# Kernel tuning notes

Hardware: AMD Instinct MI355X
Metric: run time of the kernel (lower is better)

## Reference

```python
import jax, jax.numpy as jnp
import numpy as np

CONF_THRES = 0.5
IOU_THRES = 0.4
MAX_DET = 100
MAX_WH = 1024.0
K_NMS = 4096  # static cap on NMS candidates (>> expected #candidates passing conf_thres)


def setup_inputs() -> dict:
    key = jax.random.key(0)
    k1, k2, k3, k4 = jax.random.split(key, 4)
    bs, gs, nc = 16, 25200, 80  # YOLOv5 @ 640x640: 25200 anchors, 80 classes, ps = 85
    xy = jax.random.uniform(k1, (bs, gs, 2)) * 608.0 + 16.0   # centers in [16, 624)
    wh = jax.random.uniform(k2, (bs, gs, 2)) * 96.0 + 4.0     # sizes in [4, 100)
    obj = jax.random.uniform(k3, (bs, gs, 1))                 # objectness
    cls = jax.random.uniform(k4, (bs, gs, nc)) * 0.505        # class probs; obj*cls > 0.5 is rare (~1-2k hits)
    prediction = jnp.concatenate([xy, wh, obj, cls], axis=-1)  # [bs, gs, 85]
    return {"prediction": prediction}


def _postprocess(prediction):
    bs, gs, ps = prediction.shape
    nc = ps - 5
    p = prediction.reshape(-1, ps)                 # [N, ps], N = bs*gs
    obj = p[:, 4]                                  # objectness
    scores_all = p[:, 5:] * obj[:, None]           # conf = cls * obj, [N, nc]
    # candidate (anchor, class) pairs: obj > conf_thres AND conf > conf_thres (multi_label)
    cand = (obj[:, None] > CONF_THRES) & (scores_all > CONF_THRES)
    flat = jnp.where(cand, scores_all, -1.0).reshape(-1)       # [N*nc]
    top_scores, top_idx = jax.lax.top_k(flat, K_NMS)           # descending score order (= torch nms sort order)
    row = top_idx // nc                                        # anchor index into p
    cls_j = top_idx % nc                                       # class index
    batch = row // gs                                          # image index
    valid = top_scores > CONF_THRES

    # xywh -> xyxy
    xywh = p[row, :4]                                          # [K, 4]
    half = xywh[:, 2:4] * 0.5
    box = jnp.concatenate([xywh[:, 0:2] - half, xywh[:, 0:2] + half], axis=1)
    f32 = box.dtype

    # class-offset + batch-offset trick: c1 = batch*max_cls_idx*max_wh, c2 = class*max_wh
    offset = (batch.astype(f32) * (nc * MAX_WH) + cls_j.astype(f32) * MAX_WH)[:, None]
    nb = box + offset                                          # offset boxes for NMS

    # pairwise IoU [K, K]
    area = (nb[:, 2] - nb[:, 0]) * (nb[:, 3] - nb[:, 1])
    ix = jnp.maximum(jnp.minimum(nb[:, None, 2], nb[None, :, 2]) - jnp.maximum(nb[:, None, 0], nb[None, :, 0]), 0.0)
    iy = jnp.maximum(jnp.minimum(nb[:, None, 3], nb[None, :, 3]) - jnp.maximum(nb[:, None, 1], nb[None, :, 1]), 0.0)
    inter = ix * iy
    iou = inter / (area[:, None] + area[None, :] - inter)

    # greedy NMS over score-sorted candidates (torchvision semantics: suppress if IoU > thres)
    def step(supp, xs):
        iou_i, v_i, i = xs
        keep_i = v_i & jnp.logical_not(supp[i])
        supp = supp | (keep_i & (iou_i > IOU_THRES))
        return supp, keep_i
    _, keep = jax.lax.scan(step, jnp.zeros(K_NMS, bool), (iou, valid, jnp.arange(K_NMS)))

    # output rows: [x1, y1, x2, y2, conf, class, batch]
    rows7 = jnp.concatenate(
        [box, top_scores[:, None], cls_j.astype(f32)[:, None], batch.astype(f32)[:, None]], axis=1)

    # per-image gather of kept rows (score order), truncated to MAX_DET, zero-padded
    def gather_b(b):
        m = keep & (batch == b)
        rank = jnp.cumsum(m.astype(jnp.int32)) - 1
        idx = jnp.where(m & (rank < MAX_DET), rank, MAX_DET)   # overflow/invalid -> dropped slot
        buf = jnp.zeros((MAX_DET + 1, 7), f32).at[idx].set(jnp.where(m[:, None], rows7, 0.0))
        return buf[:MAX_DET]
    return jax.vmap(gather_b)(jnp.arange(bs))                  # [bs, MAX_DET, 7]


def reference(prediction):
    return _postprocess(prediction)
```

## Files before the change

kernel.cpp:

```cpp
#include <hip/hip_runtime.h>
#include <stdint.h>

#define BS 16
#define GS 25200
#define NC 80
#define PS 85
#define NROWS (BS * GS)
#define MAXDET 100
#define CAP 4096
#define NGROUPS (BS * NC)
#define RPB 64
#define SLABF (RPB * PS)
#define PPB (RPB * NC)

struct Ws {
  int      count;
  int      keep[CAP];
  float    sc[CAP];
  int      ti[CAP];
  uint16_t gg[CAP];
  float    x1[CAP];
  float    y1[CAP];
  float    x2[CAP];
  float    y2[CAP];
};

__global__ __launch_bounds__(256) void extract_k(const float* __restrict__ p,
                                                 Ws* __restrict__ w) {
  __shared__ float slab[SLABF];
  int tid = threadIdx.x;
  const float4* __restrict__ src =
      (const float4*)(p + (size_t)blockIdx.x * SLABF);
  float4* dst = (float4*)slab;
#pragma unroll
  for (int i = 0; i < 6; ++i) {
    int idx = tid + i * 256;
    if (idx < SLABF / 4) dst[idx] = src[idx];
  }
  __syncthreads();
  int lane = tid & 63;
  int rowbase = blockIdx.x * RPB;
#pragma unroll 4
  for (int step = 0; step < PPB / 256; ++step) {
    int k = tid + step * 256;
    int row = k / NC;
    int c   = k - row * NC;
    float obj = slab[row * PS + 4];
    bool hit = false;
    float s = 0.0f;
    if (obj > 0.5f) {
      s = slab[row * PS + 5 + c] * obj;
      hit = s > 0.5f;
    }
    uint64_t mm = __ballot(hit);
    if (mm) {
      int leader = __ffsll((unsigned long long)mm) - 1;
      int pos0;
      if (lane == leader) pos0 = atomicAdd(&w->count, __popcll(mm));
      pos0 = __shfl(pos0, leader);
      if (hit) {
        int slot = pos0 + __popcll(mm & ((1ull << lane) - 1ull));
        if (slot < CAP) {
          int grow = rowbase + row;
          int b = grow / GS;
          float x = slab[row * PS + 0], y = slab[row * PS + 1];
          float hw = slab[row * PS + 2] * 0.5f, hh = slab[row * PS + 3] * 0.5f;
          w->sc[slot] = s;
          w->ti[slot] = grow * NC + c;
          w->gg[slot] = (uint16_t)(b * NC + c);
          w->x1[slot] = x - hw;
          w->y1[slot] = y - hh;
          w->x2[slot] = x + hw;
          w->y2[slot] = y + hh;
        }
      }
    }
  }
}

__global__ __launch_bounds__(256) void nms_k(Ws* __restrict__ w) {
  __shared__ uint64_t lkey[4][64];
  __shared__ int      lj[4][64];
  int wslot = threadIdx.x >> 6;
  int wid   = (blockIdx.x * 256 + threadIdx.x) >> 6;
  int lane  = threadIdx.x & 63;
  int b = wid / NC, c = wid - b * NC;
  float offf = (float)b * (NC * 1024.0f) + (float)c * 1024.0f;
  int n = w->count;
  if (n > CAP) n = CAP;
  int nm = 0;
  for (int j0 = 0; j0 < n; j0 += 64) {
    int j = j0 + lane;
    int g = (j < n) ? (int)w->gg[j] : -1;
    bool mem = (g == wid);
    uint64_t mm = __ballot(mem);
    if (!mm) continue;
    if (mem) {
      int pos = nm + __popcll(mm & ((1ull << lane) - 1ull));
      if (pos < 64) {
        uint32_t sb = __float_as_uint(w->sc[j]);
        lkey[wslot][pos] = ((uint64_t)sb << 32) | (uint32_t)(~(uint32_t)w->ti[j]);
        lj[wslot][pos]   = j;
      } else {
        w->keep[j] = 0;
      }
    }
    nm += __popcll(mm);
  }
  __syncthreads();
  if (nm > 64) nm = 64;
  if (nm == 0) return;
  uint64_t key = (lane < nm) ? lkey[wslot][lane] : 0ull;
  int      jv  = (lane < nm) ? lj[wslot][lane] : -1;
  for (int k = 2; k <= 64; k <<= 1) {
    for (int s = k >> 1; s > 0; s >>= 1) {
      uint64_t ok = __shfl_xor(key, s);
      int      oj = __shfl_xor(jv, s);
      bool iLow       = (lane & s) == 0;
      bool descRun    = (lane & k) == 0;
      bool wantLarger = (iLow == descRun);
      bool take = wantLarger ? (ok > key) : (ok < key);
      if (take) { key = ok; jv = oj; }
    }
  }
  float kx1 = 0.f, ky1 = 0.f, kx2 = 0.f, ky2 = 0.f, ka = 0.f;
  int nk = 0;
  for (int i = 0; i < nm; ++i) {
    int jm = __shfl(jv, i);
    float cx1 = w->x1[jm] + offf;
    float cy1 = w->y1[jm] + offf;
    float cx2 = w->x2[jm] + offf;
    float cy2 = w->y2[jm] + offf;
    float car = (cx2 - cx1) * (cy2 - cy1);
    bool over = false;
    if (lane < nk) {
      float ix = fmaxf(fminf(kx2, cx2) - fmaxf(kx1, cx1), 0.0f);
      float iy = fmaxf(fminf(ky2, cy2) - fmaxf(ky1, cy1), 0.0f);
      float inter = ix * iy;
      over = inter / (ka + car - inter) > 0.4f;
    }
    bool kept = !__any(over);
    if (kept) {
      if (lane == nk) { kx1 = cx1; ky1 = cy1; kx2 = cx2; ky2 = cy2; ka = car; }
      ++nk;
    }
    if (lane == 0) w->keep[jm] = kept ? 1 : 0;
  }
}

__global__ __launch_bounds__(1024) void gather_k(const Ws* __restrict__ w,
                                                 float* __restrict__ out) {
  __shared__ uint64_t skey[BS][256];
  __shared__ int      sj[BS][256];
  int wvb  = threadIdx.x >> 6;
  int lane = threadIdx.x & 63;
  int glo = wvb * NC;
  int n = w->count;
  if (n > CAP) n = CAP;
  int nkept = 0;
  for (int j0 = 0; j0 < n; j0 += 64) {
    int j = j0 + lane;
    bool m = false;
    if (j < n) {
      int g = (int)w->gg[j];
      m = ((unsigned)(g - glo) < (unsigned)NC) && (w->keep[j] != 0);
    }
    uint64_t mm = __ballot(m);
    if (m) {
      int pos = nkept + __popcll(mm & ((1ull << lane) - 1ull));
      if (pos < 256) {
        uint32_t sb = __float_as_uint(w->sc[j]);
        skey[wvb][pos] = ((uint64_t)sb << 32) | (uint32_t)(~(uint32_t)w->ti[j]);
        sj[wvb][pos]   = j;
      }
    }
    nkept += __popcll(mm);
  }
  if (nkept > 256) nkept = 256;
  for (int e = lane; e < 256; e += 64)
    if (e >= nkept) { skey[wvb][e] = 0ull; sj[wvb][e] = -1; }
  __syncthreads();
  for (int k = 2; k <= 256; k <<= 1) {
    for (int s = k >> 1; s > 0; s >>= 1) {
      for (int e = lane; e < 256; e += 64) {
        int x = e ^ s;
        if (x > e) {
          uint64_t a = skey[wvb][e], bb = skey[wvb][x];
          bool desc = (e & k) == 0;
          if (desc ? (a < bb) : (a > bb)) {
            skey[wvb][e] = bb; skey[wvb][x] = a;
            int t = sj[wvb][e]; sj[wvb][e] = sj[wvb][x]; sj[wvb][x] = t;
          }
        }
      }
      __syncthreads();
    }
  }
  int nout = nkept < MAXDET ? nkept : MAXDET;
  float* ob = out + (size_t)wvb * MAXDET * 7;
  for (int i = lane; i < MAXDET; i += 64) {
    if (i < nout) {
      int j = sj[wvb][i];
      ob[i * 7 + 0] = w->x1[j];
      ob[i * 7 + 1] = w->y1[j];
      ob[i * 7 + 2] = w->x2[j];
      ob[i * 7 + 3] = w->y2[j];
      ob[i * 7 + 4] = w->sc[j];
      ob[i * 7 + 5] = (float)((int)w->gg[j] - glo);
      ob[i * 7 + 6] = (float)wvb;
    } else {
      for (int q = 0; q < 7; ++q) ob[i * 7 + q] = 0.0f;
    }
  }
}

extern "C" void kernel_launch(void* const* d_in, const int* in_sizes, int n_in,
                              void* d_out, int out_size, void* d_ws,
                              size_t ws_size, hipStream_t stream) {
  const float* p = (const float*)d_in[0];
  float* out = (float*)d_out;
  Ws* w = (Ws*)d_ws;

  hipMemsetAsync(&w->count, 0, sizeof(int), stream);
  hipLaunchKernelGGL(extract_k, dim3(NROWS / RPB), dim3(256), 0, stream, p, w);
  hipLaunchKernelGGL(nms_k, dim3(NGROUPS / 4), dim3(256), 0, stream, w);
  hipLaunchKernelGGL(gather_k, dim3(1), dim3(1024), 0, stream, w, out);
}
```

Before: 97.10 us.

## Read predictions directly from global memory and batch hit compaction per wave

```diff
diff --git a/kernel.cpp b/kernel.cpp
--- a/kernel.cpp
+++ b/kernel.cpp
@@ -9,9 +9,8 @@
 #define MAXDET 100
 #define CAP 4096
 #define NGROUPS (BS * NC)
-#define RPB 64
-#define SLABF (RPB * PS)
-#define PPB (RPB * NC)
+#define PPB (64 * NC)
+#define STEPS (PPB / 256)
 
 struct Ws {
   int      count;
@@ -27,53 +26,57 @@
 
 __global__ __launch_bounds__(256) void extract_k(const float* __restrict__ p,
                                                  Ws* __restrict__ w) {
-  __shared__ float slab[SLABF];
-  int tid = threadIdx.x;
-  const float4* __restrict__ src =
-      (const float4*)(p + (size_t)blockIdx.x * SLABF);
-  float4* dst = (float4*)slab;
+  int tid  = threadIdx.x;
+  int lane = tid & 63;
+  uint32_t kbase = blockIdx.x * PPB + tid;
+  uint32_t hitmask = 0;
 #pragma unroll
-  for (int i = 0; i < 6; ++i) {
-    int idx = tid + i * 256;
-    if (idx < SLABF / 4) dst[idx] = src[idx];
-  }
-  __syncthreads();
-  int lane = tid & 63;
-  int rowbase = blockIdx.x * RPB;
-#pragma unroll 4
-  for (int step = 0; step < PPB / 256; ++step) {
-    int k = tid + step * 256;
-    int row = k / NC;
-    int c   = k - row * NC;
-    float obj = slab[row * PS + 4];
-    bool hit = false;
-    float s = 0.0f;
+  for (int s = 0; s < STEPS; ++s) {
+    uint32_t k   = kbase + s * 256;
+    uint32_t row = k / NC;
+    uint32_t c   = k - row * NC;
+    float obj = p[(size_t)row * PS + 4];
     if (obj > 0.5f) {
-      s = slab[row * PS + 5 + c] * obj;
-      hit = s > 0.5f;
-    }
-    uint64_t mm = __ballot(hit);
-    if (mm) {
-      int leader = __ffsll((unsigned long long)mm) - 1;
-      int pos0;
-      if (lane == leader) pos0 = atomicAdd(&w->count, __popcll(mm));
-      pos0 = __shfl(pos0, leader);
-      if (hit) {
-        int slot = pos0 + __popcll(mm & ((1ull << lane) - 1ull));
-        if (slot < CAP) {
-          int grow = rowbase + row;
-          int b = grow / GS;
-          float x = slab[row * PS + 0], y = slab[row * PS + 1];
-          float hw = slab[row * PS + 2] * 0.5f, hh = slab[row * PS + 3] * 0.5f;
-          w->sc[slot] = s;
-          w->ti[slot] = grow * NC + c;
-          w->gg[slot] = (uint16_t)(b * NC + c);
-          w->x1[slot] = x - hw;
-          w->y1[slot] = y - hh;
-          w->x2[slot] = x + hw;
-          w->y2[slot] = y + hh;
-        }
-      }
+      float sc = p[(size_t)row * PS + 5 + c] * obj;
+      if (sc > 0.5f) hitmask |= (1u << s);
+    }
+  }
+  if (__any(hitmask != 0)) {
+    int nh = __popc(hitmask);
+    int incl = nh;
+#pragma unroll
+    for (int d = 1; d < 64; d <<= 1) {
+      int o = __shfl_up(incl, d);
+      if (lane >= d) incl += o;
+    }
+    int total = __shfl(incl, 63);
+    int base = 0;
+    if (lane == 63) base = atomicAdd(&w->count, total);
+    base = __shfl(base, 63);
+    int slot = base + incl - nh;
+    uint32_t m = hitmask;
+    while (m) {
+      int s = __ffs(m) - 1;
+      m &= m - 1;
+      if (slot < CAP) {
+        uint32_t k   = kbase + (uint32_t)s * 256;
+        uint32_t row = k / NC;
+        uint32_t c   = k - row * NC;
+        const float* pr = p + (size_t)row * PS;
+        float obj = pr[4];
+        float sc  = pr[5 + c] * obj;
+        float x = pr[0], y = pr[1];
+        float hw = pr[2] * 0.5f, hh = pr[3] * 0.5f;
+        int b = row / GS;
+        w->sc[slot] = sc;
+        w->ti[slot] = (int)k;
+        w->gg[slot] = (uint16_t)(b * NC + (int)c);
+        w->x1[slot] = x - hw;
+        w->y1[slot] = y - hh;
+        w->x2[slot] = x + hw;
+        w->y2[slot] = y + hh;
+      }
+      ++slot;
     }
   }
 }
@@ -222,7 +225,7 @@
   Ws* w = (Ws*)d_ws;
 
   hipMemsetAsync(&w->count, 0, sizeof(int), stream);
-  hipLaunchKernelGGL(extract_k, dim3(NROWS / RPB), dim3(256), 0, stream, p, w);
+  hipLaunchKernelGGL(extract_k, dim3(NROWS / 64), dim3(256), 0, stream, p, w);
   hipLaunchKernelGGL(nms_k, dim3(NGROUPS / 4), dim3(256), 0, stream, w);
   hipLaunchKernelGGL(gather_k, dim3(1), dim3(1024), 0, stream, w, out);
 }
```

Result: slower. 112.5 us (+15.8%).
